# Performance work log

Hardware: AMD Instinct MI355X
Metric: run time of the kernel (lower is better)

The kernel has to match this reference:

```python
import jax, jax.numpy as jnp
import numpy as np

# ---- constants derived exactly as in CQCCExtractor.__init__ ----
SR = 16000
FMIN = 32.7
N_BINS = 96
BINS_OCT = 24
N_CQCC = 20
HOP = 128
Q = 1.0 / (2.0 ** (1.0 / BINS_OCT) - 1.0)
MIN_WIN = max(16, int(Q * SR / FMIN))          # 16699
N_FFT = 1
while N_FFT < MIN_WIN * 2:
    N_FFT <<= 1                                # 65536
NUM_FREQ = N_FFT // 2 + 1                      # 32769


def _dct_mat():
    k = np.arange(N_CQCC)[:, None]
    n = np.arange(N_BINS)[None, :]
    return jnp.asarray(np.cos(np.pi * k * (2 * n + 1) / (2 * N_BINS)), dtype=jnp.float32)


def _delta(feat, N=2):
    # vectorized version of the per-frame python loop: d[t] = sum_n n*(f[min(t+n,T-1)] - f[max(t-n,0)]) / denom
    denom = 2 * sum(i * i for i in range(1, N + 1))
    T = feat.shape[0]
    p = jnp.concatenate([jnp.repeat(feat[:1], N, axis=0), feat, jnp.repeat(feat[-1:], N, axis=0)], axis=0)
    num = sum(n * (p[N + n:N + n + T] - p[N - n:N - n + T]) for n in range(1, N + 1))
    return num / denom


def setup_inputs() -> dict:
    key = jax.random.key(0)
    wav = jax.random.normal(key, (262144,), dtype=jnp.float32)
    return {"wav": wav}


def reference(wav) -> jnp.ndarray:
    # periodic hann window of length MIN_WIN, zero-padded (centered) to N_FFT like torch.stft
    w = 0.5 - 0.5 * jnp.cos(2.0 * jnp.pi * jnp.arange(MIN_WIN, dtype=jnp.float32) / MIN_WIN)
    left = (N_FFT - MIN_WIN) // 2
    win = jnp.zeros((N_FFT,), dtype=jnp.float32).at[left:left + MIN_WIN].set(w)

    # torch.stft(center=True, pad_mode='reflect')
    pad = N_FFT // 2
    x = jnp.pad(wav, pad, mode='reflect')
    n_frames = 1 + wav.shape[0] // HOP
    starts = jnp.arange(n_frames) * HOP
    frames = x[starts[:, None] + jnp.arange(N_FFT)[None, :]] * win      # [T, n_fft]
    spec = jnp.fft.rfft(frames, axis=-1)                                 # [T, F] complex64
    power = jnp.abs(spec) ** 2                                           # [T, F]

    # linear interpolation of STFT power at geometrically spaced CQT freqs
    cqt_freqs = FMIN * 2.0 ** (jnp.arange(N_BINS, dtype=jnp.float32) / BINS_OCT)
    idx_float = cqt_freqs / (SR / 2) * (NUM_FREQ - 1)
    idx_lo = jnp.clip(idx_float.astype(jnp.int32), 0, NUM_FREQ - 2)
    idx_hi = idx_lo + 1
    alpha = (idx_float - idx_lo.astype(jnp.float32))                     # [n_bins]
    cqt_power = (1.0 - alpha) * power[:, idx_lo] + alpha * power[:, idx_hi]  # [T, n_bins]

    log_cqt = jnp.log(jnp.maximum(cqt_power, 1e-8))
    cqcc = log_cqt @ _dct_mat().T                                        # [T, n_cqcc]
    # normalize over time (torch.std default is unbiased, ddof=1)
    cqcc = (cqcc - cqcc.mean(axis=0)) / (jnp.std(cqcc, axis=0, ddof=1) + 1e-8)

    d1 = _delta(cqcc)
    d2 = _delta(d1)
    return jnp.concatenate([cqcc, d1, d2], axis=-1)                      # [T, 3*n_cqcc]
```

## Files before the change

kernel.cpp:

```cpp
#include <hip/hip_runtime.h>
#include <math.h>

#define WAV_N     262144
#define HOP       128
#define MIN_WIN   16699
#define LEFT      24418
#define T_FRAMES  2049
#define N_BINS    96
#define N_CQCC    20
#define F_COMP    192
#define NF        576
#define NBLK      2179
#define NBP       2240
#define PARTLEN   59
#define FULLBLK   130
#define XS_VALID  278843
#define TWOPI     6.283185307179586f

#define BT   64
#define FTW  32
#define JC   32
#define AST  68

#define WS_QFP  0
#define WS_SC   20643840
#define WS_CQ   23801856
#define WS_SUMS 23965776
#define SCP     2056

__device__ __forceinline__ void f_to_fi_sigma(int f, int& fi, int& sigma) {
    int plane = f / 192;
    int c = f - plane * 192;
    int bin = c >> 1, hi = c & 1;
    float e    = (float)bin / 24.0f;
    float fb   = 32.7f * exp2f(e);
    float idxf = fb / 8000.0f * 32768.0f;
    fi = (int)idxf + hi;
    sigma = (plane == 0) ? 0 : (plane == 1 ? 1 : -1);
}

__global__ __launch_bounds__(256) void k_chunk(const float* __restrict__ wav,
                                               float4* __restrict__ QFP) {
    __shared__ float A_lds[JC * AST];
    int tid = threadIdx.x;
    int b0 = blockIdx.x * BT;
    int f0 = blockIdx.y * FTW;
    int ftp = tid & 15;
    int bg  = tid >> 4;
    int bb  = b0 + bg * 4;

    int fi[2], sg[2];
    f_to_fi_sigma(f0 + 2 * ftp,     fi[0], sg[0]);
    f_to_fi_sigma(f0 + 2 * ftp + 1, fi[1], sg[1]);

    float Dr[2], Di[2];
    #pragma unroll
    for (int h = 0; h < 2; ++h) {
        float fr = (float)fi[h] * (1.0f / 65536.0f)
                 - (float)sg[h] * (1.0f / (float)MIN_WIN);
        fr -= rintf(fr);
        float sn, cs; __sincosf(TWOPI * fr, &sn, &cs);
        Dr[h] = cs; Di[h] = -sn;
    }

    float xr[2][4], xi[2][4], pr[2][4], pi[2][4];
    #pragma unroll
    for (int h = 0; h < 2; ++h)
        #pragma unroll
        for (int i = 0; i < 4; ++i) { xr[h][i] = 0.f; xi[h][i] = 0.f; }

    for (int jc = 0; jc < 4; ++jc) {
        int jbase = jc * JC;
        __syncthreads();
        #pragma unroll
        for (int i = 0; i < 8; ++i) {
            int m = i * 256 + tid;
            int j = m & 31, bl = m >> 5;
            int s = 128 * (b0 + bl) + jbase + j;
            float v = 0.0f;
            if (s < XS_VALID) {
                int w = s - 8350;
                if (w < 0) w = -w;
                if (w >= WAV_N) w = 2 * WAV_N - 2 - w;
                v = wav[w];
            }
            A_lds[j * AST + bl] = v;
        }
        __syncthreads();
        float Wr[2], Wi[2];
        #pragma unroll
        for (int h = 0; h < 2; ++h) {
            float fr = (float)((jbase * fi[h]) & 65535) * (1.0f / 65536.0f)
                     - (float)sg[h] * (float)jbase * (1.0f / (float)MIN_WIN);
            fr -= rintf(fr);
            float sn, cs; __sincosf(TWOPI * fr, &sn, &cs);
            Wr[h] = cs; Wi[h] = -sn;
        }
        #pragma unroll 8
        for (int j32 = 0; j32 < JC; ++j32) {
            if (jc == 1 && j32 == PARTLEN - 32) {
                #pragma unroll
                for (int h = 0; h < 2; ++h)
                    #pragma unroll
                    for (int i = 0; i < 4; ++i) { pr[h][i] = xr[h][i]; pi[h][i] = xi[h][i]; }
            }
            float4 a = *(const float4*)&A_lds[j32 * AST + bg * 4];
            const float aa[4] = {a.x, a.y, a.z, a.w};
            #pragma unroll
            for (int h = 0; h < 2; ++h) {
                float wr = Wr[h], wi = Wi[h];
                #pragma unroll
                for (int i = 0; i < 4; ++i) {
                    xr[h][i] = fmaf(aa[i], wr, xr[h][i]);
                    xi[h][i] = fmaf(aa[i], wi, xi[h][i]);
                }
                Wr[h] = wr * Dr[h] - wi * Di[h];
                Wi[h] = wr * Di[h] + wi * Dr[h];
            }
        }
    }

    #pragma unroll
    for (int h = 0; h < 2; ++h) {
        int f = f0 + 2 * ftp + h;
        float4* dst = QFP + (size_t)f * NBP + bb;
        #pragma unroll
        for (int i = 0; i < 4; ++i) {
            int b = bb + i;
            unsigned ph = ((unsigned)fi[h] * (unsigned)(LEFT + 128 * b)) & 65535u;
            float frf = (float)ph * (1.0f / 65536.0f)
                      - (float)sg[h] * (float)((128 * b) % MIN_WIN) * (1.0f / (float)MIN_WIN);
            frf -= rintf(frf);
            float sn, cs; __sincosf(TWOPI * frf, &sn, &cs);
            dst[i] = make_float4(xr[h][i] * cs + xi[h][i] * sn,
                                 xi[h][i] * cs - xr[h][i] * sn,
                                 pr[h][i] * cs + pi[h][i] * sn,
                                 pi[h][i] * cs - pr[h][i] * sn);
        }
    }
}

#define SEG 9
__global__ __launch_bounds__(256) void k_scan(const float4* __restrict__ QFP,
                                              float2* __restrict__ Sc,
                                              double* __restrict__ sums) {
    __shared__ float2 col[3 * NBLK];
    __shared__ double2 wsum[3][4];
    int tid = threadIdx.x;
    int c = blockIdx.x;
    if (c == 0 && tid < 40) sums[tid] = 0.0;

    const float2* base = (const float2*)QFP;
    #pragma unroll
    for (int p = 0; p < 3; ++p) {
        size_t foff = (size_t)(p * 192 + c) * NBP;
        #pragma unroll
        for (int k = 0; k < SEG; ++k) {
            int idx = k * 256 + tid;
            if (idx < NBLK) col[p * NBLK + idx] = base[2 * (foff + idx)];
        }
    }
    __syncthreads();

    int s0 = tid * SEG, s1 = min(s0 + SEG, NBLK);
    double sr[3] = {0, 0, 0}, si[3] = {0, 0, 0};
    #pragma unroll
    for (int p = 0; p < 3; ++p)
        for (int i = s0; i < s1; ++i) {
            sr[p] += col[p * NBLK + i].x;
            si[p] += col[p * NBLK + i].y;
        }
    double r[3], im[3];
    #pragma unroll
    for (int p = 0; p < 3; ++p) { r[p] = sr[p]; im[p] = si[p]; }
    #pragma unroll
    for (int off = 1; off < 64; off <<= 1) {
        #pragma unroll
        for (int p = 0; p < 3; ++p) {
            double prx = __shfl_up(r[p], off);
            double piy = __shfl_up(im[p], off);
            if ((tid & 63) >= off) { r[p] += prx; im[p] += piy; }
        }
    }
    if ((tid & 63) == 63) {
        #pragma unroll
        for (int p = 0; p < 3; ++p) wsum[p][tid >> 6] = make_double2(r[p], im[p]);
    }
    __syncthreads();
    int w = tid >> 6;
    double gr[3], gi[3];
    #pragma unroll
    for (int p = 0; p < 3; ++p) {
        double basr = 0.0, basi = 0.0;
        for (int ww = 0; ww < w; ++ww) { basr += wsum[p][ww].x; basi += wsum[p][ww].y; }
        gr[p] = basr + r[p] - sr[p];
        gi[p] = basi + im[p] - si[p];
    }
    for (int i = s0; i < s1; ++i) {
        #pragma unroll
        for (int p = 0; p < 3; ++p) {
            float2 old = col[p * NBLK + i];
            col[p * NBLK + i] = make_float2((float)gr[p], (float)gi[p]);
            gr[p] += old.x; gi[p] += old.y;
        }
    }
    __syncthreads();

    int fi_[3], sg_[3];
    #pragma unroll
    for (int p = 0; p < 3; ++p) f_to_fi_sigma(p * 192 + c, fi_[p], sg_[p]);
    #pragma unroll
    for (int k = 0; k < SEG; ++k) {
        int t = k * 256 + tid;
        if (t < T_FRAMES) {
            float accx = 0.0f, accy = 0.0f;
            #pragma unroll
            for (int p = 0; p < 3; ++p) {
                float2 g0 = col[p * NBLK + t];
                float2 g1 = col[p * NBLK + t + FULLBLK];
                float2 qp = base[2 * ((size_t)(p * 192 + c) * NBP + t + FULLBLK) + 1];
                float ur = g1.x - g0.x + qp.x;
                float ui = g1.y - g0.y + qp.y;
                unsigned ph = ((unsigned)fi_[p] * 128u * (unsigned)t) & 65535u;
                float frf = (float)ph * (1.0f / 65536.0f)
                          - (float)sg_[p] * (float)((128 * t) % MIN_WIN) * (1.0f / (float)MIN_WIN);
                frf -= rintf(frf);
                float sn, cs;
                __sincosf(TWOPI * frf, &sn, &cs);
                float vr = ur * cs - ui * sn;
                float vi = ur * sn + ui * cs;
                float wgt = (p == 0) ? 0.5f : -0.25f;
                accx = fmaf(wgt, vr, accx);
                accy = fmaf(wgt, vi, accy);
            }
            Sc[(size_t)c * SCP + t] = make_float2(accx, accy);
        }
    }
}

__global__ __launch_bounds__(256) void k_cqt(const float2* __restrict__ Sc,
                                             float* __restrict__ cq,
                                             double* __restrict__ sums) {
    __shared__ float dctm[N_CQCC * N_BINS];
    __shared__ float lg[8][N_BINS];
    __shared__ float cqv[8][N_CQCC];
    int tid = threadIdx.x;
    int tb = blockIdx.x * 8;
    for (int idx = tid; idx < N_CQCC * N_BINS; idx += 256) {
        int k = idx / N_BINS, b = idx - k * N_BINS;
        dctm[idx] = cosf((float)M_PI * (float)(k * (2 * b + 1)) / 192.0f);
    }
    int lt = tid >> 5, lane = tid & 31;
    int t = tb + lt;
    #pragma unroll
    for (int bb = 0; bb < 3; ++bb) {
        int b = lane + 32 * bb;
        float lv = 0.0f;
        if (t < T_FRAMES) {
            float2 lo = Sc[(size_t)(2 * b) * SCP + t];
            float2 hi = Sc[(size_t)(2 * b + 1) * SCP + t];
            float pl = lo.x * lo.x + lo.y * lo.y;
            float ph = hi.x * hi.x + hi.y * hi.y;
            float e    = (float)b / 24.0f;
            float fb   = 32.7f * exp2f(e);
            float idxf = fb / 8000.0f * 32768.0f;
            float alpha = idxf - (float)((int)idxf);
            float p = (1.0f - alpha) * pl + alpha * ph;
            lv = logf(fmaxf(p, 1e-8f));
        }
        lg[lt][b] = lv;
    }
    __syncthreads();
    if (tid < 8 * N_CQCC) {
        int lt2 = tid / N_CQCC, k = tid - lt2 * N_CQCC;
        int t2 = tb + lt2;
        float s = 0.0f;
        #pragma unroll 4
        for (int b = 0; b < N_BINS; ++b) s += dctm[k * N_BINS + b] * lg[lt2][b];
        cqv[lt2][k] = (t2 < T_FRAMES) ? s : 0.0f;
        if (t2 < T_FRAMES) cq[t2 * N_CQCC + k] = s;
    }
    __syncthreads();
    if (tid < N_CQCC) {
        double s1 = 0.0, s2 = 0.0;
        #pragma unroll
        for (int lt2 = 0; lt2 < 8; ++lt2) {
            if (tb + lt2 < T_FRAMES) {
                double v = (double)cqv[lt2][tid];
                s1 += v; s2 += v * v;
            }
        }
        atomicAdd(&sums[tid], s1);
        atomicAdd(&sums[N_CQCC + tid], s2);
    }
}

__device__ __forceinline__ int clampT(int v) {
    return v < 0 ? 0 : (v > T_FRAMES - 1 ? T_FRAMES - 1 : v);
}

__global__ void k_final(const float* __restrict__ cq, const double* __restrict__ sums,
                        float* __restrict__ out) {
    int gid = blockIdx.x * blockDim.x + threadIdx.x;
    if (gid >= T_FRAMES * N_CQCC) return;
    int t = gid / N_CQCC;
    int k = gid - t * N_CQCC;
    double S1 = sums[k], S2 = sums[N_CQCC + k];
    double md = S1 / (double)T_FRAMES;
    double var = (S2 - S1 * md) / (double)(T_FRAMES - 1);
    double sd = sqrt(var > 0.0 ? var : 0.0);
    float m = (float)md;
    float iv = (float)(1.0 / (sd + 1e-8));
    float cv[9];
    #pragma unroll
    for (int j = 0; j < 9; ++j)
        cv[j] = (cq[clampT(t + j - 4) * N_CQCC + k] - m) * iv;
    float dv[5];
    #pragma unroll
    for (int o = -2; o <= 2; ++o) {
        int p = clampT(t + o);
        int h1 = clampT(p + 1) - t, l1 = clampT(p - 1) - t;
        int h2 = clampT(p + 2) - t, l2 = clampT(p - 2) - t;
        dv[o + 2] = ((cv[h1 + 4] - cv[l1 + 4]) + 2.0f * (cv[h2 + 4] - cv[l2 + 4])) * 0.1f;
    }
    out[t * 60 + k]      = cv[4];
    out[t * 60 + 20 + k] = dv[2];
    out[t * 60 + 40 + k] = (dv[3] - dv[1] + 2.0f * (dv[4] - dv[0])) * 0.1f;
}

extern "C" void kernel_launch(void* const* d_in, const int* in_sizes, int n_in,
                              void* d_out, int out_size, void* d_ws, size_t ws_size,
                              hipStream_t stream) {
    const float* wav = (const float*)d_in[0];
    float* out = (float*)d_out;
    char* ws = (char*)d_ws;
    float4* QFP  = (float4*)(ws + WS_QFP);
    float2* Sc   = (float2*)(ws + WS_SC);
    float*  cq   = (float*)(ws + WS_CQ);
    double* sums = (double*)(ws + WS_SUMS);

    k_chunk<<<dim3(NBP / BT, NF / FTW), 256, 0, stream>>>(wav, QFP);
    k_scan<<<F_COMP, 256, 0, stream>>>(QFP, Sc, sums);
    k_cqt<<<(T_FRAMES + 7) / 8, 256, 0, stream>>>(Sc, cq, sums);
    k_final<<<(T_FRAMES * N_CQCC + 255) / 256, 256, 0, stream>>>(cq, sums, out);
}
```

Baseline: 114.8 us.

## Restructure chunk kernel to one frequency per thread with single full LDS load

The chunk kernel now loads all 128 samples for a 32-block tile into LDS once, with a single barrier, instead of four 32-sample chunks with per-chunk twiddle recomputation. Each thread handles one frequency and four blocks (previously two frequencies and four blocks), and the partial-sum snapshot moves to a split loop instead of a conditional inside the inner loop. This removes repeated syncs and branch checks, but halves the block tile (BT 64 to 32), doubling grid size and lowering reuse of each LDS sample across frequencies per thread. The twiddle recurrence now runs over 128 steps without re-seeding, which may accumulate slightly more rounding error.

```diff
diff --git a/kernel.cpp b/kernel.cpp
--- a/kernel.cpp
+++ b/kernel.cpp
@@ -17,10 +17,9 @@
 #define XS_VALID  278843
 #define TWOPI     6.283185307179586f
 
-#define BT   64
+#define BT   32
 #define FTW  32
-#define JC   32
-#define AST  68
+#define AST  34
 
 #define WS_QFP  0
 #define WS_SC   20643840
@@ -41,42 +40,18 @@
 
 __global__ __launch_bounds__(256) void k_chunk(const float* __restrict__ wav,
                                                float4* __restrict__ QFP) {
-    __shared__ float A_lds[JC * AST];
+    __shared__ float A_lds[128 * AST];
     int tid = threadIdx.x;
     int b0 = blockIdx.x * BT;
     int f0 = blockIdx.y * FTW;
-    int ftp = tid & 15;
-    int bg  = tid >> 4;
-    int bb  = b0 + bg * 4;
-
-    int fi[2], sg[2];
-    f_to_fi_sigma(f0 + 2 * ftp,     fi[0], sg[0]);
-    f_to_fi_sigma(f0 + 2 * ftp + 1, fi[1], sg[1]);
-
-    float Dr[2], Di[2];
-    #pragma unroll
-    for (int h = 0; h < 2; ++h) {
-        float fr = (float)fi[h] * (1.0f / 65536.0f)
-                 - (float)sg[h] * (1.0f / (float)MIN_WIN);
-        fr -= rintf(fr);
-        float sn, cs; __sincosf(TWOPI * fr, &sn, &cs);
-        Dr[h] = cs; Di[h] = -sn;
-    }
-
-    float xr[2][4], xi[2][4], pr[2][4], pi[2][4];
-    #pragma unroll
-    for (int h = 0; h < 2; ++h)
-        #pragma unroll
-        for (int i = 0; i < 4; ++i) { xr[h][i] = 0.f; xi[h][i] = 0.f; }
-
-    for (int jc = 0; jc < 4; ++jc) {
-        int jbase = jc * JC;
-        __syncthreads();
-        #pragma unroll
-        for (int i = 0; i < 8; ++i) {
-            int m = i * 256 + tid;
-            int j = m & 31, bl = m >> 5;
-            int s = 128 * (b0 + bl) + jbase + j;
+
+    {
+        int sbase = 128 * b0;
+        #pragma unroll
+        for (int k = 0; k < 16; ++k) {
+            int m = k * 256 + tid;
+            int j = m & 127, bl = m >> 7;
+            int s = sbase + m;
             float v = 0.0f;
             if (s < XS_VALID) {
                 int w = s - 8350;
@@ -86,57 +61,74 @@
             }
             A_lds[j * AST + bl] = v;
         }
-        __syncthreads();
-        float Wr[2], Wi[2];
-        #pragma unroll
-        for (int h = 0; h < 2; ++h) {
-            float fr = (float)((jbase * fi[h]) & 65535) * (1.0f / 65536.0f)
-                     - (float)sg[h] * (float)jbase * (1.0f / (float)MIN_WIN);
-            fr -= rintf(fr);
-            float sn, cs; __sincosf(TWOPI * fr, &sn, &cs);
-            Wr[h] = cs; Wi[h] = -sn;
-        }
-        #pragma unroll 8
-        for (int j32 = 0; j32 < JC; ++j32) {
-            if (jc == 1 && j32 == PARTLEN - 32) {
-                #pragma unroll
-                for (int h = 0; h < 2; ++h)
-                    #pragma unroll
-                    for (int i = 0; i < 4; ++i) { pr[h][i] = xr[h][i]; pi[h][i] = xi[h][i]; }
-            }
-            float4 a = *(const float4*)&A_lds[j32 * AST + bg * 4];
-            const float aa[4] = {a.x, a.y, a.z, a.w};
-            #pragma unroll
-            for (int h = 0; h < 2; ++h) {
-                float wr = Wr[h], wi = Wi[h];
-                #pragma unroll
-                for (int i = 0; i < 4; ++i) {
-                    xr[h][i] = fmaf(aa[i], wr, xr[h][i]);
-                    xi[h][i] = fmaf(aa[i], wi, xi[h][i]);
-                }
-                Wr[h] = wr * Dr[h] - wi * Di[h];
-                Wi[h] = wr * Di[h] + wi * Dr[h];
-            }
-        }
-    }
-
-    #pragma unroll
-    for (int h = 0; h < 2; ++h) {
-        int f = f0 + 2 * ftp + h;
-        float4* dst = QFP + (size_t)f * NBP + bb;
+    }
+
+    int f  = f0 + (tid & 31);
+    int bg = tid >> 5;
+    int bl0 = bg * 4;
+    int bb = b0 + bl0;
+
+    int fi, sg;
+    f_to_fi_sigma(f, fi, sg);
+
+    float Dr, Di;
+    {
+        float fr = (float)fi * (1.0f / 65536.0f) - (float)sg * (1.0f / (float)MIN_WIN);
+        fr -= rintf(fr);
+        float sn, cs; __sincosf(TWOPI * fr, &sn, &cs);
+        Dr = cs; Di = -sn;
+    }
+    float Wr = 1.0f, Wi = 0.0f;
+
+    float xr[4] = {0, 0, 0, 0}, xi[4] = {0, 0, 0, 0};
+    float pr[4], pi[4];
+
+    __syncthreads();
+
+    #pragma unroll 4
+    for (int j = 0; j < PARTLEN; ++j) {
+        float2 a01 = *(const float2*)&A_lds[j * AST + bl0];
+        float2 a23 = *(const float2*)&A_lds[j * AST + bl0 + 2];
+        const float aa[4] = {a01.x, a01.y, a23.x, a23.y};
         #pragma unroll
         for (int i = 0; i < 4; ++i) {
-            int b = bb + i;
-            unsigned ph = ((unsigned)fi[h] * (unsigned)(LEFT + 128 * b)) & 65535u;
-            float frf = (float)ph * (1.0f / 65536.0f)
-                      - (float)sg[h] * (float)((128 * b) % MIN_WIN) * (1.0f / (float)MIN_WIN);
-            frf -= rintf(frf);
-            float sn, cs; __sincosf(TWOPI * frf, &sn, &cs);
-            dst[i] = make_float4(xr[h][i] * cs + xi[h][i] * sn,
-                                 xi[h][i] * cs - xr[h][i] * sn,
-                                 pr[h][i] * cs + pi[h][i] * sn,
-                                 pi[h][i] * cs - pr[h][i] * sn);
-        }
+            xr[i] = fmaf(aa[i], Wr, xr[i]);
+            xi[i] = fmaf(aa[i], Wi, xi[i]);
+        }
+        float wr = Wr;
+        Wr = wr * Dr - Wi * Di;
+        Wi = wr * Di + Wi * Dr;
+    }
+    #pragma unroll
+    for (int i = 0; i < 4; ++i) { pr[i] = xr[i]; pi[i] = xi[i]; }
+    #pragma unroll 4
+    for (int j = PARTLEN; j < 128; ++j) {
+        float2 a01 = *(const float2*)&A_lds[j * AST + bl0];
+        float2 a23 = *(const float2*)&A_lds[j * AST + bl0 + 2];
+        const float aa[4] = {a01.x, a01.y, a23.x, a23.y};
+        #pragma unroll
+        for (int i = 0; i < 4; ++i) {
+            xr[i] = fmaf(aa[i], Wr, xr[i]);
+            xi[i] = fmaf(aa[i], Wi, xi[i]);
+        }
+        float wr = Wr;
+        Wr = wr * Dr - Wi * Di;
+        Wi = wr * Di + Wi * Dr;
+    }
+
+    float4* dst = QFP + (size_t)f * NBP + bb;
+    #pragma unroll
+    for (int i = 0; i < 4; ++i) {
+        int b = bb + i;
+        unsigned ph = ((unsigned)fi * (unsigned)(LEFT + 128 * b)) & 65535u;
+        float frf = (float)ph * (1.0f / 65536.0f)
+                  - (float)sg * (float)((128 * b) % MIN_WIN) * (1.0f / (float)MIN_WIN);
+        frf -= rintf(frf);
+        float sn, cs; __sincosf(TWOPI * frf, &sn, &cs);
+        dst[i] = make_float4(xr[i] * cs + xi[i] * sn,
+                             xi[i] * cs - xr[i] * sn,
+                             pr[i] * cs + pi[i] * sn,
+                             pi[i] * cs - pr[i] * sn);
     }
 }
 
```

Result: faster. 108.2 us (-5.7%).
